# Kernel tuning notes

Hardware: AMD Instinct MI355X
Metric: run time of the kernel (lower is better)

The kernel has to match this reference:

```python
import jax, jax.numpy as jnp
import numpy as np

N = 100000      # num nodes
E = 1000000     # num edges
D_IN = 64
D_OUT = 64


def setup_inputs() -> dict:
    key = jax.random.key(0)
    k1, k2, k3, k4 = jax.random.split(key, 4)
    x = jax.random.normal(k1, (N, D_IN), dtype=jnp.float32)
    edge_index = jax.random.randint(k2, (2, E), 0, N, dtype=jnp.int32)
    weight = jax.random.normal(k3, (D_OUT, D_IN), dtype=jnp.float32) / np.float32(np.sqrt(D_IN))
    bias = jax.random.normal(k4, (D_OUT,), dtype=jnp.float32) * 0.01
    return {"x": x, "edge_index": edge_index, "weight": weight, "bias": bias}


def reference(x, edge_index, weight, bias):
    # GCNConv forward: remove self loops (as weight-0 edges for static shapes),
    # add self loops, symmetric degree normalization, linear, gather-scatter aggregate.
    n = x.shape[0]
    src, dst = edge_index[0], edge_index[1]
    keep = (src != dst).astype(x.dtype)          # filtered self-loops get weight 0
    loop = jnp.arange(n, dtype=src.dtype)
    row = jnp.concatenate([src, loop])           # [E+N] source (gather) index
    col = jnp.concatenate([dst, loop])           # [E+N] destination (scatter) index
    ew = jnp.concatenate([keep, jnp.ones((n,), x.dtype)])

    deg = jax.ops.segment_sum(ew, col, num_segments=n)            # [N]
    dis = jnp.where(deg > 0, jax.lax.rsqrt(deg), 0.0)             # deg^-0.5, inf->0
    norm = dis[row] * ew * dis[col]                               # [E+N]

    h = x @ weight.T                                              # [N, D_OUT]
    msgs = norm[:, None] * h[row]                                 # [E+N, D_OUT]
    out = jax.ops.segment_sum(msgs, col, num_segments=n)          # [N, D_OUT]
    return out + bias
```

## Files before the change

kernel.cpp:

```cpp
#include <hip/hip_runtime.h>
#include <hip/hip_bf16.h>

static constexpr int N = 100000;
static constexpr int E = 1000000;
static constexpr int D = 64;
static constexpr int NB = 391;
static constexpr int CAP = 3072;
static constexpr int PART_EPT = 8;
static constexpr int PART_CHUNK = 256 * PART_EPT;
static constexpr int PART_BLOCKS = (E + PART_CHUNK - 1) / PART_CHUNK;
static constexpr int LIN_BLOCKS = (N + 63) / 64;

typedef __attribute__((ext_vector_type(8))) short bf16x8;
typedef __attribute__((ext_vector_type(4))) float f32x4;

__device__ inline ushort f2bf(float f) {
    unsigned u = __float_as_uint(f);
    return (ushort)((u + 0x7fffu + ((u >> 16) & 1u)) >> 16);
}

__global__ __launch_bounds__(256) void k_init(const float* __restrict__ w,
                                              int* __restrict__ gcur,
                                              float* __restrict__ dis,
                                              ushort* __restrict__ wbf,
                                              ushort* __restrict__ hb) {
    int tid = threadIdx.x;
    int i0 = tid * 16;
#pragma unroll
    for (int c = 0; c < 4; ++c) {
        float4 v = *reinterpret_cast<const float4*>(w + i0 + c * 4);
        ushort4 o;
        o.x = f2bf(v.x); o.y = f2bf(v.y); o.z = f2bf(v.z); o.w = f2bf(v.w);
        *reinterpret_cast<ushort4*>(wbf + i0 + c * 4) = o;
    }
    for (int b = tid; b < NB; b += 256) gcur[b] = 0;
    if (tid == 0) dis[N] = 0.f;
    if (tid < 32) reinterpret_cast<int*>(hb + N * D)[tid] = 0;
}

__global__ __launch_bounds__(256) void k_partlin(const int* __restrict__ ei,
                                                 const float* __restrict__ x,
                                                 const ushort* __restrict__ wbf,
                                                 int* __restrict__ gcur,
                                                 int* __restrict__ part,
                                                 ushort* __restrict__ hb) {
    __shared__ int hcnt[NB];
    __shared__ int hcur[NB];
    int tid = threadIdx.x;
    if (blockIdx.x < PART_BLOCKS) {
        for (int b = tid; b < NB; b += 256) hcnt[b] = 0;
        __syncthreads();
        int base = blockIdx.x * PART_CHUNK + tid;
        int ss[PART_EPT], tt[PART_EPT];
#pragma unroll
        for (int k = 0; k < PART_EPT; ++k) {
            int i = base + k * 256;
            int s = -1, t = 0;
            if (i < E) {
                s = ei[i];
                t = ei[E + i];
                if (s == t) s = -1;
            }
            ss[k] = s; tt[k] = t;
            if (s >= 0) atomicAdd(&hcnt[t >> 8], 1);
        }
        __syncthreads();
        for (int b = tid; b < NB; b += 256) {
            int c = hcnt[b];
            hcur[b] = b * CAP + (c ? atomicAdd(&gcur[b], c) : 0);
        }
        __syncthreads();
#pragma unroll
        for (int k = 0; k < PART_EPT; ++k) {
            int s = ss[k];
            if (s >= 0) {
                int b = tt[k] >> 8;
                int pos = atomicAdd(&hcur[b], 1);
                if (pos < (b + 1) * CAP)
                    part[pos] = s | ((tt[k] & 255) << 17);
            }
        }
    } else {
        int lane = tid & 63, wave = tid >> 6;
        int tbase = (blockIdx.x - PART_BLOCKS) * 64 + wave * 16;
        if (tbase >= N) return;
        int r15 = lane & 15, g4 = lane >> 4;
        int arow = tbase + r15;
        if (arow >= N) arow = N - 1;
        bf16x8 afr[2];
#pragma unroll
        for (int ks = 0; ks < 2; ++ks) {
            const float* ap = x + arow * 64 + ks * 32 + g4 * 8;
            float4 v0 = *reinterpret_cast<const float4*>(ap);
            float4 v1 = *reinterpret_cast<const float4*>(ap + 4);
            bf16x8 a;
            a[0] = (short)f2bf(v0.x); a[1] = (short)f2bf(v0.y);
            a[2] = (short)f2bf(v0.z); a[3] = (short)f2bf(v0.w);
            a[4] = (short)f2bf(v1.x); a[5] = (short)f2bf(v1.y);
            a[6] = (short)f2bf(v1.z); a[7] = (short)f2bf(v1.w);
            afr[ks] = a;
        }
        f32x4 acc[4] = {};
#pragma unroll
        for (int nt = 0; nt < 4; ++nt)
#pragma unroll
            for (int ks = 0; ks < 2; ++ks) {
                bf16x8 b = *reinterpret_cast<const bf16x8*>(
                    wbf + (nt * 16 + r15) * 64 + ks * 32 + g4 * 8);
                acc[nt] = __builtin_amdgcn_mfma_f32_16x16x32_bf16(afr[ks], b, acc[nt], 0, 0, 0);
            }
#pragma unroll
        for (int r = 0; r < 4; ++r) {
            int node = tbase + g4 * 4 + r;
            if (node < N) {
#pragma unroll
                for (int nt = 0; nt < 4; ++nt)
                    hb[node * D + nt * 16 + r15] = f2bf(acc[nt][r]);
            }
        }
    }
}

__global__ __launch_bounds__(512) void k_csr(const int* __restrict__ gcur,
                                             const int* __restrict__ part,
                                             int2* __restrict__ rc,
                                             int* __restrict__ srcs,
                                             float* __restrict__ dis) {
    __shared__ int cntL[256];
    __shared__ int scanL[256];
    __shared__ int curL[256];
    int tid = threadIdx.x;
    int b = blockIdx.x;
    if (tid < 256) cntL[tid] = 0;
    __syncthreads();
    int en = gcur[b];
    en = en < CAP ? en : CAP;
    const int* pb = part + b * CAP;
    for (int i = tid; i < en; i += 512)
        atomicAdd(&cntL[pb[i] >> 17], 1);
    __syncthreads();
    if (tid < 256) scanL[tid] = cntL[tid];
    __syncthreads();
    for (int off = 1; off < 256; off <<= 1) {
        int v = 0;
        if (tid < 256 && tid >= off) v = scanL[tid - off];
        __syncthreads();
        if (tid < 256) scanL[tid] += v;
        __syncthreads();
    }
    if (tid < 256) {
        int node = b * 256 + tid;
        int excl = scanL[tid] - cntL[tid];
        if (node < N) {
            rc[node] = make_int2(b * CAP + excl, cntL[tid]);
            dis[node] = rsqrtf((float)(cntL[tid] + 1));
        }
        curL[tid] = excl;
    }
    __syncthreads();
    for (int i = tid; i < en; i += 512) {
        int e = pb[i];
        int pos = atomicAdd(&curL[e >> 17], 1);
        srcs[b * CAP + pos] = e & 0x1FFFF;
    }
}

#define FMACC8(d, v)                                                        \
    acc[0] = fmaf(d, __uint_as_float(((unsigned)(v).x) << 16), acc[0]);     \
    acc[1] = fmaf(d, __uint_as_float(((unsigned)(v).x) & 0xffff0000u), acc[1]); \
    acc[2] = fmaf(d, __uint_as_float(((unsigned)(v).y) << 16), acc[2]);     \
    acc[3] = fmaf(d, __uint_as_float(((unsigned)(v).y) & 0xffff0000u), acc[3]); \
    acc[4] = fmaf(d, __uint_as_float(((unsigned)(v).z) << 16), acc[4]);     \
    acc[5] = fmaf(d, __uint_as_float(((unsigned)(v).z) & 0xffff0000u), acc[5]); \
    acc[6] = fmaf(d, __uint_as_float(((unsigned)(v).w) << 16), acc[6]);     \
    acc[7] = fmaf(d, __uint_as_float(((unsigned)(v).w) & 0xffff0000u), acc[7]);

__global__ __launch_bounds__(256) void k_agg(const int2* __restrict__ rc,
                                             const int* __restrict__ srcs,
                                             const ushort* __restrict__ hb,
                                             const float* __restrict__ dis,
                                             const float* __restrict__ bias,
                                             float* __restrict__ out) {
    int g = blockIdx.x * 256 + threadIdx.x;
    int t = g >> 6, lane = g & 63;
    if (t >= N) return;
    int q = lane >> 3, l = lane & 7;
    int2 bc = rc[t];
    int base = bc.x, len = bc.y;

    int lb = lane & 7;
    int4 vt = *reinterpret_cast<const int4*>(hb + t * D + lb * 8);
    float4 ba = *reinterpret_cast<const float4*>(&bias[lb * 8]);
    float4 bb = *reinterpret_cast<const float4*>(&bias[lb * 8 + 4]);
    float dt = rsqrtf((float)(len + 1));

    float acc[8];
#pragma unroll
    for (int i = 0; i < 8; ++i) acc[i] = 0.f;

    int s0 = (q < len) ? srcs[base + q] : N;
    int s1 = (8 + q < len) ? srcs[base + 8 + q] : N;
    float d0 = dis[s0];
    int4  v0 = *reinterpret_cast<const int4*>(hb + s0 * D + l * 8);
    float d1 = dis[s1];
    int4  v1 = *reinterpret_cast<const int4*>(hb + s1 * D + l * 8);
    for (int k0 = 16; k0 < len; k0 += 8) {
        int idx = k0 + q;
        int s2 = (idx < len) ? srcs[base + idx] : N;
        float d2 = dis[s2];
        int4  v2 = *reinterpret_cast<const int4*>(hb + s2 * D + l * 8);
        FMACC8(d0, v0);
        d0 = d1; v0 = v1;
        d1 = d2; v1 = v2;
    }
    FMACC8(d0, v0);
    FMACC8(d1, v1);

#pragma unroll
    for (int i = 0; i < 8; ++i) {
        acc[i] += __shfl_down(acc[i], 32);
        acc[i] += __shfl_down(acc[i], 16);
        acc[i] += __shfl_down(acc[i], 8);
    }
    if (lane < 8) {
        FMACC8(dt, vt);
        float4 o0, o1;
        o0.x = fmaf(dt, acc[0], ba.x);
        o0.y = fmaf(dt, acc[1], ba.y);
        o0.z = fmaf(dt, acc[2], ba.z);
        o0.w = fmaf(dt, acc[3], ba.w);
        o1.x = fmaf(dt, acc[4], bb.x);
        o1.y = fmaf(dt, acc[5], bb.y);
        o1.z = fmaf(dt, acc[6], bb.z);
        o1.w = fmaf(dt, acc[7], bb.w);
        *reinterpret_cast<float4*>(out + t * D + lane * 8) = o0;
        *reinterpret_cast<float4*>(out + t * D + lane * 8 + 4) = o1;
    }
}

extern "C" void kernel_launch(void* const* d_in, const int* in_sizes, int n_in,
                              void* d_out, int out_size, void* d_ws, size_t ws_size,
                              hipStream_t stream) {
    const float* x    = (const float*)d_in[0];
    const int*   ei   = (const int*)d_in[1];
    const float* w    = (const float*)d_in[2];
    const float* bias = (const float*)d_in[3];
    float* out = (float*)d_out;

    char* ws = (char*)d_ws;
    int*    gcur = (int*)(ws);
    ushort* wbf  = (ushort*)(ws + 1664);
    int*    part = (int*)(ws + 9856);
    int*    srcs = (int*)(ws + 4814464);
    int2*   rc   = (int2*)(ws + 9619072);
    float*  dis  = (float*)(ws + 10419072);
    ushort* hb   = (ushort*)(ws + 10819200);

    k_init   <<<1, 256, 0, stream>>>(w, gcur, dis, wbf, hb);
    k_partlin<<<PART_BLOCKS + LIN_BLOCKS, 256, 0, stream>>>(ei, x, wbf, gcur, part, hb);
    k_csr    <<<NB, 512, 0, stream>>>(gcur, part, rc, srcs, dis);
    k_agg    <<<(N * 64) / 256, 256, 0, stream>>>(rc, srcs, hb, dis, bias, out);
}
```

Baseline: 78.48 us.

## Remap aggregation lanes to 32 dims x 2 edges with 4-byte gathers

The aggregation kernel changes its lane mapping. Previously eight lanes covered a 64-dim row with 16-byte loads, eight edges per step, with a three-level shuffle reduction. Now 32 lanes cover the row with 4-byte bf16-pair loads and two edges run in parallel, each lane keeping four independent loads in flight per stage in a two-stage pipeline. This cuts register accumulators and the shuffle reduction to one step, at the cost of more, smaller load instructions per row and more index and dis loads per lane.

```diff
diff --git a/kernel.cpp b/kernel.cpp
--- a/kernel.cpp
+++ b/kernel.cpp
@@ -165,15 +165,16 @@
     }
 }
 
-#define FMACC8(d, v)                                                        \
-    acc[0] = fmaf(d, __uint_as_float(((unsigned)(v).x) << 16), acc[0]);     \
-    acc[1] = fmaf(d, __uint_as_float(((unsigned)(v).x) & 0xffff0000u), acc[1]); \
-    acc[2] = fmaf(d, __uint_as_float(((unsigned)(v).y) << 16), acc[2]);     \
-    acc[3] = fmaf(d, __uint_as_float(((unsigned)(v).y) & 0xffff0000u), acc[3]); \
-    acc[4] = fmaf(d, __uint_as_float(((unsigned)(v).z) << 16), acc[4]);     \
-    acc[5] = fmaf(d, __uint_as_float(((unsigned)(v).z) & 0xffff0000u), acc[5]); \
-    acc[6] = fmaf(d, __uint_as_float(((unsigned)(v).w) << 16), acc[6]);     \
-    acc[7] = fmaf(d, __uint_as_float(((unsigned)(v).w) & 0xffff0000u), acc[7]);
+#define LDE(ii, dv, vv)                                                     \
+    {                                                                       \
+        int _i = (ii);                                                      \
+        int _s = (_i < len) ? srcs[base + _i] : N;        \
+        dv = dis[_s];                                                       \
+        vv = hb32[_s * 32 + dl];                                            \
+    }
+#define CONS(dv, vv)                                                        \
+    acc0 = fmaf(dv, __uint_as_float((vv) << 16), acc0);                     \
+    acc1 = fmaf(dv, __uint_as_float((vv) & 0xffff0000u), acc1);
 
 __global__ __launch_bounds__(256) void k_agg(const int2* __restrict__ rc,
                                              const int* __restrict__ srcs,
@@ -184,57 +185,57 @@
     int g = blockIdx.x * 256 + threadIdx.x;
     int t = g >> 6, lane = g & 63;
     if (t >= N) return;
-    int q = lane >> 3, l = lane & 7;
+    int half = lane >> 5, dl = lane & 31;
+    const unsigned* hb32 = reinterpret_cast<const unsigned*>(hb);
     int2 bc = rc[t];
     int base = bc.x, len = bc.y;
 
-    int lb = lane & 7;
-    int4 vt = *reinterpret_cast<const int4*>(hb + t * D + lb * 8);
-    float4 ba = *reinterpret_cast<const float4*>(&bias[lb * 8]);
-    float4 bb = *reinterpret_cast<const float4*>(&bias[lb * 8 + 4]);
     float dt = rsqrtf((float)(len + 1));
-
-    float acc[8];
-#pragma unroll
-    for (int i = 0; i < 8; ++i) acc[i] = 0.f;
-
-    int s0 = (q < len) ? srcs[base + q] : N;
-    int s1 = (8 + q < len) ? srcs[base + 8 + q] : N;
-    float d0 = dis[s0];
-    int4  v0 = *reinterpret_cast<const int4*>(hb + s0 * D + l * 8);
-    float d1 = dis[s1];
-    int4  v1 = *reinterpret_cast<const int4*>(hb + s1 * D + l * 8);
-    for (int k0 = 16; k0 < len; k0 += 8) {
-        int idx = k0 + q;
-        int s2 = (idx < len) ? srcs[base + idx] : N;
-        float d2 = dis[s2];
-        int4  v2 = *reinterpret_cast<const int4*>(hb + s2 * D + l * 8);
-        FMACC8(d0, v0);
-        d0 = d1; v0 = v1;
-        d1 = d2; v1 = v2;
-    }
-    FMACC8(d0, v0);
-    FMACC8(d1, v1);
-
-#pragma unroll
-    for (int i = 0; i < 8; ++i) {
-        acc[i] += __shfl_down(acc[i], 32);
-        acc[i] += __shfl_down(acc[i], 16);
-        acc[i] += __shfl_down(acc[i], 8);
-    }
-    if (lane < 8) {
-        FMACC8(dt, vt);
-        float4 o0, o1;
-        o0.x = fmaf(dt, acc[0], ba.x);
-        o0.y = fmaf(dt, acc[1], ba.y);
-        o0.z = fmaf(dt, acc[2], ba.z);
-        o0.w = fmaf(dt, acc[3], ba.w);
-        o1.x = fmaf(dt, acc[4], bb.x);
-        o1.y = fmaf(dt, acc[5], bb.y);
-        o1.z = fmaf(dt, acc[6], bb.z);
-        o1.w = fmaf(dt, acc[7], bb.w);
-        *reinterpret_cast<float4*>(out + t * D + lane * 8) = o0;
-        *reinterpret_cast<float4*>(out + t * D + lane * 8 + 4) = o1;
+    unsigned vt = hb32[t * 32 + dl];
+    float2 bb = *reinterpret_cast<const float2*>(bias + 2 * dl);
+
+    float acc0 = 0.f, acc1 = 0.f;
+
+    float da0, da1, da2, da3;
+    unsigned va0, va1, va2, va3;
+    LDE(half,     da0, va0);
+    LDE(2 + half, da1, va1);
+    LDE(4 + half, da2, va2);
+    LDE(6 + half, da3, va3);
+    if (len > 8) {
+        float db0, db1, db2, db3;
+        unsigned vb0, vb1, vb2, vb3;
+        LDE(8 + half,  db0, vb0);
+        LDE(10 + half, db1, vb1);
+        LDE(12 + half, db2, vb2);
+        LDE(14 + half, db3, vb3);
+        for (int k0 = 16; k0 < len; k0 += 8) {
+            float dc0, dc1, dc2, dc3;
+            unsigned vc0, vc1, vc2, vc3;
+            LDE(k0 + half,     dc0, vc0);
+            LDE(k0 + 2 + half, dc1, vc1);
+            LDE(k0 + 4 + half, dc2, vc2);
+            LDE(k0 + 6 + half, dc3, vc3);
+            CONS(da0, va0); CONS(da1, va1); CONS(da2, va2); CONS(da3, va3);
+            da0 = db0; va0 = vb0; da1 = db1; va1 = vb1;
+            da2 = db2; va2 = vb2; da3 = db3; va3 = vb3;
+            db0 = dc0; vb0 = vc0; db1 = dc1; vb1 = vc1;
+            db2 = dc2; vb2 = vc2; db3 = dc3; vb3 = vc3;
+        }
+        CONS(da0, va0); CONS(da1, va1); CONS(da2, va2); CONS(da3, va3);
+        CONS(db0, vb0); CONS(db1, vb1); CONS(db2, vb2); CONS(db3, vb3);
+    } else {
+        CONS(da0, va0); CONS(da1, va1); CONS(da2, va2); CONS(da3, va3);
+    }
+
+    acc0 += __shfl_down(acc0, 32);
+    acc1 += __shfl_down(acc1, 32);
+    if (lane < 32) {
+        CONS(dt, vt);
+        float2 o;
+        o.x = fmaf(dt, acc0, bb.x);
+        o.y = fmaf(dt, acc1, bb.y);
+        *reinterpret_cast<float2*>(out + t * D + 2 * dl) = o;
     }
 }
 
```

After: 97.94 us. 1.25x slower.
